# Kernel tuning notes

Hardware: AMD Instinct MI355X
Metric: run time of the kernel (lower is better)

Reference implementation:

```python
import jax, jax.numpy as jnp
import numpy as np

EPS = 1e-5
B, N, K = 2, 40960, 16
D_OUT = 64
H = D_OUT // 2  # 32

PNAMES = ['mlp1_w','mlp1_b','mlp1_g','mlp1_beta','mlp1_m','mlp1_v',
          'ap1_fc_w','ap1_fc_b','ap1_mlp_w','ap1_mlp_b','ap1_g','ap1_beta','ap1_m','ap1_v',
          'mlp2_w','mlp2_b','mlp2_g','mlp2_beta','mlp2_m','mlp2_v',
          'ap2_fc_w','ap2_fc_b','ap2_mlp_w','ap2_mlp_b','ap2_g','ap2_beta','ap2_m','ap2_v']


def _conv1x1(x, w, b):
    # x: (B,C,N,K), w: (O,C) -> (B,O,N,K)
    return jnp.einsum('oc,bcnk->bonk', w, x) + b[None, :, None, None]


def _bn(x, g, beta, m, v):
    # eval-mode BatchNorm2d over channel axis 1
    scale = g / jnp.sqrt(v + EPS)
    return (x - m[None, :, None, None]) * scale[None, :, None, None] + beta[None, :, None, None]


def _gather_neighbour(pc, idx):
    # pc: (B,N,d), idx: (B,N,K) -> (B,N,K,d)
    b, n, d = pc.shape
    k = idx.shape[-1]
    flat = idx.reshape(b, n * k)
    feats = jnp.take_along_axis(pc, flat[:, :, None], axis=1)  # (B,N*K,d)
    return feats.reshape(b, n, k, d)


def _rel_pos_enc(xyz, idx):
    nbr = _gather_neighbour(xyz, idx)                       # (B,N,K,3)
    tile = jnp.broadcast_to(xyz[:, :, None, :], nbr.shape)  # (B,N,K,3)
    rel = tile - nbr
    dist = jnp.sqrt(jnp.sum(rel * rel, axis=-1, keepdims=True))
    return jnp.concatenate([dist, rel, tile, nbr], axis=-1)  # (B,N,K,10)


def _att_pool(f, fc_w, fc_b, mw, mb, g, beta, m, v):
    # f: (B,C,N,K)
    att = jax.nn.relu(_conv1x1(f, fc_w, fc_b))
    scores = jax.nn.softmax(att, axis=3)
    agg = jnp.sum(f * scores, axis=3, keepdims=True)        # (B,C,N,1)
    return jax.nn.relu(_bn(_conv1x1(agg, mw, mb), g, beta, m, v))


def _forward(xyz, feature, neigh_idx, p):
    # relative pos encoding -> (B,10,N,K)
    f_xyz = _rel_pos_enc(xyz, neigh_idx).transpose(0, 3, 1, 2)
    f_xyz = jax.nn.relu(_bn(_conv1x1(f_xyz, p['mlp1_w'], p['mlp1_b']),
                            p['mlp1_g'], p['mlp1_beta'], p['mlp1_m'], p['mlp1_v']))  # (B,H,N,K)
    f_nb = _gather_neighbour(feature[..., 0].transpose(0, 2, 1), neigh_idx).transpose(0, 3, 1, 2)  # (B,H,N,K)
    f_cat = jnp.concatenate([f_nb, f_xyz], axis=1)          # (B,D_OUT,N,K)
    f_agg = _att_pool(f_cat, p['ap1_fc_w'], p['ap1_fc_b'], p['ap1_mlp_w'], p['ap1_mlp_b'],
                      p['ap1_g'], p['ap1_beta'], p['ap1_m'], p['ap1_v'])  # (B,H,N,1)
    f_xyz = jax.nn.relu(_bn(_conv1x1(f_xyz, p['mlp2_w'], p['mlp2_b']),
                            p['mlp2_g'], p['mlp2_beta'], p['mlp2_m'], p['mlp2_v']))  # (B,H,N,K)
    f_nb = _gather_neighbour(f_agg[..., 0].transpose(0, 2, 1), neigh_idx).transpose(0, 3, 1, 2)  # (B,H,N,K)
    f_cat = jnp.concatenate([f_nb, f_xyz], axis=1)          # (B,D_OUT,N,K)
    return _att_pool(f_cat, p['ap2_fc_w'], p['ap2_fc_b'], p['ap2_mlp_w'], p['ap2_mlp_b'],
                     p['ap2_g'], p['ap2_beta'], p['ap2_m'], p['ap2_v'])  # (B,D_OUT,N,1)


def setup_inputs() -> dict:
    key = jax.random.key(0)
    ks = iter(jax.random.split(key, 64))

    def w(o, c):
        return jax.random.normal(next(ks), (o, c), jnp.float32) * float(np.sqrt(2.0 / c))

    def bias(c):
        return jax.random.normal(next(ks), (c,), jnp.float32) * 0.01

    def bnp(c):
        g = jax.random.uniform(next(ks), (c,), jnp.float32, 0.5, 1.5)
        beta = jax.random.normal(next(ks), (c,), jnp.float32) * 0.1
        m = jax.random.normal(next(ks), (c,), jnp.float32) * 0.1
        v = jax.random.uniform(next(ks), (c,), jnp.float32, 0.5, 1.5)
        return g, beta, m, v

    inp = {}
    inp['xyz'] = jax.random.normal(next(ks), (B, N, 3), jnp.float32)
    inp['feature'] = jax.random.normal(next(ks), (B, H, N, 1), jnp.float32)
    inp['mlp1_w'], inp['mlp1_b'] = w(H, 10), bias(H)
    inp['mlp1_g'], inp['mlp1_beta'], inp['mlp1_m'], inp['mlp1_v'] = bnp(H)
    inp['ap1_fc_w'], inp['ap1_fc_b'] = w(D_OUT, D_OUT), bias(D_OUT)
    inp['ap1_mlp_w'], inp['ap1_mlp_b'] = w(H, D_OUT), bias(H)
    inp['ap1_g'], inp['ap1_beta'], inp['ap1_m'], inp['ap1_v'] = bnp(H)
    inp['mlp2_w'], inp['mlp2_b'] = w(H, H), bias(H)
    inp['mlp2_g'], inp['mlp2_beta'], inp['mlp2_m'], inp['mlp2_v'] = bnp(H)
    inp['ap2_fc_w'], inp['ap2_fc_b'] = w(D_OUT, D_OUT), bias(D_OUT)
    inp['ap2_mlp_w'], inp['ap2_mlp_b'] = w(D_OUT, D_OUT), bias(D_OUT)
    inp['ap2_g'], inp['ap2_beta'], inp['ap2_m'], inp['ap2_v'] = bnp(D_OUT)
    inp['neigh_idx'] = jax.random.randint(next(ks), (B, N, K), 0, N, jnp.int64 if jax.config.jax_enable_x64 else jnp.int32)
    return inp


def reference(xyz, feature, mlp1_w, mlp1_b, mlp1_g, mlp1_beta, mlp1_m, mlp1_v,
              ap1_fc_w, ap1_fc_b, ap1_mlp_w, ap1_mlp_b, ap1_g, ap1_beta, ap1_m, ap1_v,
              mlp2_w, mlp2_b, mlp2_g, mlp2_beta, mlp2_m, mlp2_v,
              ap2_fc_w, ap2_fc_b, ap2_mlp_w, ap2_mlp_b, ap2_g, ap2_beta, ap2_m, ap2_v,
              neigh_idx):
    p = dict(zip(PNAMES, (mlp1_w, mlp1_b, mlp1_g, mlp1_beta, mlp1_m, mlp1_v,
                          ap1_fc_w, ap1_fc_b, ap1_mlp_w, ap1_mlp_b, ap1_g, ap1_beta, ap1_m, ap1_v,
                          mlp2_w, mlp2_b, mlp2_g, mlp2_beta, mlp2_m, mlp2_v,
                          ap2_fc_w, ap2_fc_b, ap2_mlp_w, ap2_mlp_b, ap2_g, ap2_beta, ap2_m, ap2_v)))
    return _forward(xyz, feature, neigh_idx, p)
```

## Files before the change

kernel.cpp:

```cpp
#include <hip/hip_runtime.h>
#include <math.h>

#define BB 2
#define NN 40960
#define KK 16

typedef float v2f __attribute__((ext_vector_type(2)));
typedef _Float16 h16;
typedef h16 h16x2 __attribute__((ext_vector_type(2)));

__device__ __forceinline__ v2f fma2(v2f a, v2f b, v2f c){
  return __builtin_elementwise_fma(a, b, c);
}
__device__ __forceinline__ v2f mk2(float a, float b){ v2f r; r.x=a; r.y=b; return r; }

#if __has_builtin(__builtin_amdgcn_fdot2)
__device__ __forceinline__ float dot2acc(h16x2 w, h16x2 f, float acc){
  return __builtin_amdgcn_fdot2(w, f, acc, false);
}
#else
__device__ __forceinline__ float dot2acc(h16x2 w, h16x2 f, float acc){
  return acc + (float)w.x*(float)f.x + (float)w.y*(float)f.y;
}
#endif
#if __has_builtin(__builtin_amdgcn_exp2f)
__device__ __forceinline__ float exp2fast(float x){ return __builtin_amdgcn_exp2f(x); }
#else
__device__ __forceinline__ float exp2fast(float x){ return __expf(x*0.6931471805599453f); }
#endif
#if __has_builtin(__builtin_amdgcn_cvt_pkrtz)
__device__ __forceinline__ h16x2 pkh(float a, float b){
  return __builtin_bit_cast(h16x2, __builtin_amdgcn_cvt_pkrtz(a,b));
}
#else
__device__ __forceinline__ h16x2 pkh(float a, float b){ h16x2 r; r.x=(h16)a; r.y=(h16)b; return r; }
#endif

template<int CTRL>
__device__ __forceinline__ float dppf(float x){
  return __int_as_float(__builtin_amdgcn_update_dpp(0, __float_as_int(x), CTRL, 0xF, 0xF, true));
}
__device__ __forceinline__ float red16_sum(float v){
  v += dppf<0xB1>(v);
  v += dppf<0x4E>(v);
  v += dppf<0x141>(v);
  v += dppf<0x140>(v);
  return v;
}

__device__ alignas(16) float g_pw1[32*10];
__device__ alignas(16) float g_pb1[32];
__device__ alignas(16) h16x2 g_w2h[32*16];
__device__ alignas(16) float g_pb2[32];
__device__ alignas(16) h16x2 g_fch1[64*32];
__device__ alignas(16) float g_fcb1s[64];
__device__ alignas(16) h16x2 g_fch2[64*32];
__device__ alignas(16) float g_fcb2s[64];
__device__ alignas(16) float g_pcw[32*64];
__device__ alignas(16) float g_pcb[32];
__device__ alignas(16) float g_pdw[64*64];
__device__ alignas(16) float g_pdb[64];

#define LOG2E 1.44269504088896f

__global__ __launch_bounds__(256) void k_pre(
  const float* __restrict__ feat, float* __restrict__ feat_t,
  const float* __restrict__ w1, const float* __restrict__ b1,
  const float* __restrict__ g1, const float* __restrict__ be1, const float* __restrict__ m1, const float* __restrict__ v1,
  const float* __restrict__ fc1w, const float* __restrict__ fc1b,
  const float* __restrict__ cw, const float* __restrict__ cb,
  const float* __restrict__ cg, const float* __restrict__ cbe, const float* __restrict__ cm, const float* __restrict__ cv,
  const float* __restrict__ w2, const float* __restrict__ b2,
  const float* __restrict__ g2, const float* __restrict__ be2, const float* __restrict__ m2, const float* __restrict__ v2,
  const float* __restrict__ fc2w, const float* __restrict__ fc2b,
  const float* __restrict__ dw, const float* __restrict__ db,
  const float* __restrict__ dg, const float* __restrict__ dbe, const float* __restrict__ dm, const float* __restrict__ dv)
{
  int tid = threadIdx.x;
  int bid = blockIdx.x;
  if (bid < BB*NN/256){
    int b = bid / (NN/256);
    int n = (bid % (NN/256))*256 + tid;
    float v[32];
    #pragma unroll
    for (int h=0; h<32; ++h) v[h] = feat[((size_t)(b*32+h))*NN + n];
    float* o = feat_t + ((size_t)b*NN + n)*32;
    #pragma unroll
    for (int h=0; h<32; h+=4){ *(float4*)(o+h) = make_float4(v[h],v[h+1],v[h+2],v[h+3]); }
    return;
  }
  for (int i=tid; i<320; i+=256){ int h=i/10;
    g_pw1[i] = w1[i] * (g1[h]*rsqrtf(v1[h]+1e-5f)); }
  if (tid<32){ float s=g1[tid]*rsqrtf(v1[tid]+1e-5f);
    g_pb1[tid] = (b1[tid]-m1[tid])*s+be1[tid]; }
  for (int i=tid; i<512; i+=256){ int h=i>>4, c=i&15;
    float s=g2[h]*rsqrtf(v2[h]+1e-5f);
    g_w2h[i] = pkh(w2[h*32+2*c]*s, w2[h*32+2*c+1]*s); }
  if (tid<32){ float s=g2[tid]*rsqrtf(v2[tid]+1e-5f);
    g_pb2[tid] = (b2[tid]-m2[tid])*s+be2[tid]; }
  for (int i=tid; i<2048; i+=256){ int o=i>>5, c=i&31;
    g_fch1[i] = pkh(fc1w[o*64+2*c]*LOG2E, fc1w[o*64+2*c+1]*LOG2E);
    g_fch2[i] = pkh(fc2w[o*64+2*c]*LOG2E, fc2w[o*64+2*c+1]*LOG2E); }
  if (tid<64){ g_fcb1s[tid] = fc1b[tid]*LOG2E; g_fcb2s[tid] = fc2b[tid]*LOG2E; }
  for (int i=tid; i<2048; i+=256){ int h=i>>6;
    g_pcw[i] = cw[i] * (cg[h]*rsqrtf(cv[h]+1e-5f)); }
  if (tid<32){ float s=cg[tid]*rsqrtf(cv[tid]+1e-5f);
    g_pcb[tid] = (cb[tid]-cm[tid])*s+cbe[tid]; }
  for (int i=tid; i<4096; i+=256){ int h=i>>6;
    g_pdw[i] = dw[i] * (dg[h]*rsqrtf(dv[h]+1e-5f)); }
  if (tid<64){ float s=dg[tid]*rsqrtf(dv[tid]+1e-5f);
    g_pdb[tid] = (db[tid]-dm[tid])*s+dbe[tid]; }
}

__global__ __launch_bounds__(256,2) void k_stage1(
  const float* __restrict__ xyz, const float* __restrict__ feat_t, const int* __restrict__ nidx,
  float* __restrict__ fagg)
{
  int tid = threadIdx.x;
  int lane = tid & 63, wvv = tid >> 6;
  int k = lane & 15, ns = lane >> 4;
  int b = blockIdx.x / (NN/16);
  int n = (blockIdx.x % (NN/16))*16 + wvv*4 + ns;
  size_t bn = (size_t)b*NN + n;
  int idxv = nidx[bn*KK + k];

  alignas(16) float fc_[64];
  const float* fb = feat_t + ((size_t)b*NN + idxv)*32;
  #pragma unroll
  for (int h=0; h<32; h+=4){ float4 x=*(const float4*)(fb+h);
    fc_[h]=x.x; fc_[h+1]=x.y; fc_[h+2]=x.z; fc_[h+3]=x.w; }

  const float* tp = xyz + bn*3;
  const float* qp = xyz + ((size_t)b*NN + idxv)*3;
  float t0=tp[0],t1=tp[1],t2=tp[2];
  float q0=qp[0],q1=qp[1],q2=qp[2];
  float r0=t0-q0,r1=t1-q1,r2=t2-q2;
  v2f e2[5] = { {sqrtf(r0*r0+r1*r1+r2*r2), r0}, {r1,r2}, {t0,t1}, {t2,q0}, {q1,q2} };

  #pragma unroll
  for (int h=0; h<32; ++h){
    const v2f* wr = (const v2f*)(g_pw1 + h*10);
    v2f acc = mk2(g_pb1[h], 0.f);
    #pragma unroll
    for (int c=0; c<5; ++c) acc = fma2(wr[c], e2[c], acc);
    fc_[32+h] = fmaxf(acc.x+acc.y, 0.f);
  }

  h16x2 h2[32];
  #pragma unroll
  for (int c=0; c<32; ++c) h2[c] = pkh(fc_[2*c], fc_[2*c+1]);

  float sp4[4], sf4[4];
  #pragma unroll
  for (int ob=0; ob<64; ob+=4){
    const h16x2* w0 = &g_fch1[(ob+0)*32];
    const h16x2* w1p = &g_fch1[(ob+1)*32];
    const h16x2* w2p = &g_fch1[(ob+2)*32];
    const h16x2* w3p = &g_fch1[(ob+3)*32];
    float a0=g_fcb1s[ob+0], a1=g_fcb1s[ob+1], a2=g_fcb1s[ob+2], a3=g_fcb1s[ob+3];
    #pragma unroll
    for (int c=0; c<32; ++c){
      h16x2 f = h2[c];
      a0 = dot2acc(w0[c], f, a0); a1 = dot2acc(w1p[c], f, a1);
      a2 = dot2acc(w2p[c], f, a2); a3 = dot2acc(w3p[c], f, a3);
    }
    float p0=exp2fast(fmaxf(a0,0.f)), p1=exp2fast(fmaxf(a1,0.f));
    float p2=exp2fast(fmaxf(a2,0.f)), p3=exp2fast(fmaxf(a3,0.f));
    float f0=(float)h2[(ob>>1)+0].x, f1=(float)h2[(ob>>1)+0].y;
    float f2=(float)h2[(ob>>1)+1].x, f3=(float)h2[(ob>>1)+1].y;
    float q0v=f0*p0, q1v=f1*p1, q2v=f2*p2, q3v=f3*p3;
    float s0=red16_sum(p0), s1=red16_sum(p1), s2=red16_sum(p2), s3=red16_sum(p3);
    float t0v=red16_sum(q0v), t1v=red16_sum(q1v), t2v=red16_sum(q2v), t3v=red16_sum(q3v);
    if ((ob>>2)==k){
      sp4[0]=s0; sp4[1]=s1; sp4[2]=s2; sp4[3]=s3;
      sf4[0]=t0v; sf4[1]=t1v; sf4[2]=t2v; sf4[3]=t3v;
    }
  }
  v2f a01 = mk2(__fdividef(sf4[0],sp4[0]), __fdividef(sf4[1],sp4[1]));
  v2f a23 = mk2(__fdividef(sf4[2],sp4[2]), __fdividef(sf4[3],sp4[3]));

  float o0=0.f, o1=0.f;
  #pragma unroll
  for (int h=0; h<32; h+=2){
    const v2f* wr0 = (const v2f*)(g_pcw + h*64 + 4*k);
    const v2f* wr1 = (const v2f*)(g_pcw + (h+1)*64 + 4*k);
    v2f p0 = fma2(wr0[0], a01, wr0[1]*a23);
    v2f p1 = fma2(wr1[0], a01, wr1[1]*a23);
    float r0v = red16_sum(p0.x + p0.y);
    float r1v = red16_sum(p1.x + p1.y);
    float v0 = fmaxf(r0v + g_pcb[h], 0.f);
    float v1 = fmaxf(r1v + g_pcb[h+1], 0.f);
    if ((h&15)==k){ if (h<16) o0=v0; else o1=v0; }
    if (((h+1)&15)==k){ if (h+1<16) o0=v1; else o1=v1; }
  }
  float* fo = fagg + bn*32;
  fo[k]=o0; fo[k+16]=o1;
}

__global__ __launch_bounds__(256,2) void k_stage2(
  const float* __restrict__ xyz, const float* __restrict__ fagg, const int* __restrict__ nidx,
  float* __restrict__ outp)
{
  int tid = threadIdx.x;
  int lane = tid & 63, wvv = tid >> 6;
  int k = lane & 15, ns = lane >> 4;
  int b = blockIdx.x / (NN/16);
  int n = (blockIdx.x % (NN/16))*16 + wvv*4 + ns;
  size_t bn = (size_t)b*NN + n;
  int idxv = nidx[bn*KK + k];

  alignas(16) float fc_[64];
  const float* fb = fagg + ((size_t)b*NN + idxv)*32;
  #pragma unroll
  for (int h=0; h<32; h+=4){ float4 x=*(const float4*)(fb+h);
    fc_[h]=x.x; fc_[h+1]=x.y; fc_[h+2]=x.z; fc_[h+3]=x.w; }

  const float* tp = xyz + bn*3;
  const float* qp = xyz + ((size_t)b*NN + idxv)*3;
  float t0=tp[0],t1=tp[1],t2=tp[2];
  float q0=qp[0],q1=qp[1],q2=qp[2];
  float r0=t0-q0,r1=t1-q1,r2=t2-q2;
  v2f e2[5] = { {sqrtf(r0*r0+r1*r1+r2*r2), r0}, {r1,r2}, {t0,t1}, {t2,q0}, {q1,q2} };

  alignas(8) float fx[32];
  #pragma unroll
  for (int h=0; h<32; ++h){
    const v2f* wr = (const v2f*)(g_pw1 + h*10);
    v2f acc = mk2(g_pb1[h], 0.f);
    #pragma unroll
    for (int c=0; c<5; ++c) acc = fma2(wr[c], e2[c], acc);
    fx[h] = fmaxf(acc.x+acc.y, 0.f);
  }
  h16x2 hx[16];
  #pragma unroll
  for (int c=0; c<16; ++c) hx[c] = pkh(fx[2*c], fx[2*c+1]);
  #pragma unroll
  for (int h=0; h<32; h+=2){
    const h16x2* wr0 = &g_w2h[(h+0)*16];
    const h16x2* wr1 = &g_w2h[(h+1)*16];
    float a0 = g_pb2[h+0], a1 = g_pb2[h+1];
    #pragma unroll
    for (int c=0; c<16; ++c){ h16x2 f=hx[c]; a0=dot2acc(wr0[c],f,a0); a1=dot2acc(wr1[c],f,a1); }
    fc_[32+h]   = fmaxf(a0, 0.f);
    fc_[32+h+1] = fmaxf(a1, 0.f);
  }

  h16x2 h2[32];
  #pragma unroll
  for (int c=0; c<32; ++c) h2[c] = pkh(fc_[2*c], fc_[2*c+1]);

  float sp4[4], sf4[4];
  #pragma unroll
  for (int ob=0; ob<64; ob+=4){
    const h16x2* w0 = &g_fch2[(ob+0)*32];
    const h16x2* w1p = &g_fch2[(ob+1)*32];
    const h16x2* w2p = &g_fch2[(ob+2)*32];
    const h16x2* w3p = &g_fch2[(ob+3)*32];
    float a0=g_fcb2s[ob+0], a1=g_fcb2s[ob+1], a2=g_fcb2s[ob+2], a3=g_fcb2s[ob+3];
    #pragma unroll
    for (int c=0; c<32; ++c){
      h16x2 f = h2[c];
      a0 = dot2acc(w0[c], f, a0); a1 = dot2acc(w1p[c], f, a1);
      a2 = dot2acc(w2p[c], f, a2); a3 = dot2acc(w3p[c], f, a3);
    }
    float p0=exp2fast(fmaxf(a0,0.f)), p1=exp2fast(fmaxf(a1,0.f));
    float p2=exp2fast(fmaxf(a2,0.f)), p3=exp2fast(fmaxf(a3,0.f));
    float f0=(float)h2[(ob>>1)+0].x, f1=(float)h2[(ob>>1)+0].y;
    float f2=(float)h2[(ob>>1)+1].x, f3=(float)h2[(ob>>1)+1].y;
    float q0v=f0*p0, q1v=f1*p1, q2v=f2*p2, q3v=f3*p3;
    float s0=red16_sum(p0), s1=red16_sum(p1), s2=red16_sum(p2), s3=red16_sum(p3);
    float t0v=red16_sum(q0v), t1v=red16_sum(q1v), t2v=red16_sum(q2v), t3v=red16_sum(q3v);
    if ((ob>>2)==k){
      sp4[0]=s0; sp4[1]=s1; sp4[2]=s2; sp4[3]=s3;
      sf4[0]=t0v; sf4[1]=t1v; sf4[2]=t2v; sf4[3]=t3v;
    }
  }
  v2f a01 = mk2(__fdividef(sf4[0],sp4[0]), __fdividef(sf4[1],sp4[1]));
  v2f a23 = mk2(__fdividef(sf4[2],sp4[2]), __fdividef(sf4[3],sp4[3]));

  float o4[4];
  #pragma unroll
  for (int h=0; h<64; h+=2){
    const v2f* wr0 = (const v2f*)(g_pdw + h*64 + 4*k);
    const v2f* wr1 = (const v2f*)(g_pdw + (h+1)*64 + 4*k);
    v2f p0 = fma2(wr0[0], a01, wr0[1]*a23);
    v2f p1 = fma2(wr1[0], a01, wr1[1]*a23);
    float r0v = red16_sum(p0.x + p0.y);
    float r1v = red16_sum(p1.x + p1.y);
    float v0 = fmaxf(r0v + g_pdb[h], 0.f);
    float v1 = fmaxf(r1v + g_pdb[h+1], 0.f);
    if ((h&15)==k) o4[h>>4] = v0;
    if (((h+1)&15)==k) o4[(h+1)>>4] = v1;
  }
  #pragma unroll
  for (int j=0; j<4; ++j)
    outp[((size_t)(b*64 + k + 16*j))*NN + n] = o4[j];
}

extern "C" void kernel_launch(void* const* d_in, const int* in_sizes, int n_in,
                              void* d_out, int out_size, void* d_ws, size_t ws_size,
                              hipStream_t stream){
  const float* xyz     = (const float*)d_in[0];
  const float* feature = (const float*)d_in[1];
  const int*   nidx    = (const int*)d_in[30];
  float* feat_t = (float*)d_ws;
  float* fagg   = feat_t + (size_t)BB*NN*32;

  k_pre<<<BB*NN/256 + 1, 256, 0, stream>>>(feature, feat_t,
    (const float*)d_in[2],(const float*)d_in[3],(const float*)d_in[4],(const float*)d_in[5],
    (const float*)d_in[6],(const float*)d_in[7],
    (const float*)d_in[8],(const float*)d_in[9],
    (const float*)d_in[10],(const float*)d_in[11],(const float*)d_in[12],(const float*)d_in[13],
    (const float*)d_in[14],(const float*)d_in[15],
    (const float*)d_in[16],(const float*)d_in[17],(const float*)d_in[18],(const float*)d_in[19],
    (const float*)d_in[20],(const float*)d_in[21],
    (const float*)d_in[22],(const float*)d_in[23],
    (const float*)d_in[24],(const float*)d_in[25],(const float*)d_in[26],(const float*)d_in[27],
    (const float*)d_in[28],(const float*)d_in[29]);
  k_stage1<<<BB*NN/16, 256, 0, stream>>>(xyz, feat_t, nidx, fagg);
  k_stage2<<<BB*NN/16, 256, 0, stream>>>(xyz, fagg, nidx, (float*)d_out);
}
```

Baseline: 426.5 us.

## Replace DPP-reduced post-pool MLP with LDS broadcast and fp16 dot2 per-lane outputs

After attention pooling, each lane writes its four aggregated channels to shared memory. Every lane then reads back the full 64-channel vector and computes its own output channels with fp16 packed dot products. This replaces the earlier scheme of distributed partial products followed by 16-lane DPP reductions for every output channel. The post-pool weights are now stored as packed fp16, and features are packed to fp16 directly at load time. This cuts the many cross-lane reductions and register-array shuffling, but adds LDS traffic, a wave-level wait, and lower precision in the final matmul.

```diff
diff --git a/kernel.cpp b/kernel.cpp
--- a/kernel.cpp
+++ b/kernel.cpp
@@ -47,6 +47,10 @@
   v += dppf<0x140>(v);
   return v;
 }
+__device__ __forceinline__ void wave_sync(){
+  asm volatile("s_waitcnt lgkmcnt(0)" ::: "memory");
+  __builtin_amdgcn_sched_barrier(0);
+}
 
 __device__ alignas(16) float g_pw1[32*10];
 __device__ alignas(16) float g_pb1[32];
@@ -56,9 +60,9 @@
 __device__ alignas(16) float g_fcb1s[64];
 __device__ alignas(16) h16x2 g_fch2[64*32];
 __device__ alignas(16) float g_fcb2s[64];
-__device__ alignas(16) float g_pcw[32*64];
+__device__ alignas(16) h16x2 g_cwh[32*32];
 __device__ alignas(16) float g_pcb[32];
-__device__ alignas(16) float g_pdw[64*64];
+__device__ alignas(16) h16x2 g_dwh[64*32];
 __device__ alignas(16) float g_pdb[64];
 
 #define LOG2E 1.44269504088896f
@@ -102,12 +106,14 @@
     g_fch1[i] = pkh(fc1w[o*64+2*c]*LOG2E, fc1w[o*64+2*c+1]*LOG2E);
     g_fch2[i] = pkh(fc2w[o*64+2*c]*LOG2E, fc2w[o*64+2*c+1]*LOG2E); }
   if (tid<64){ g_fcb1s[tid] = fc1b[tid]*LOG2E; g_fcb2s[tid] = fc2b[tid]*LOG2E; }
-  for (int i=tid; i<2048; i+=256){ int h=i>>6;
-    g_pcw[i] = cw[i] * (cg[h]*rsqrtf(cv[h]+1e-5f)); }
+  for (int i=tid; i<1024; i+=256){ int h=i>>5, c=i&31;
+    float s=cg[h]*rsqrtf(cv[h]+1e-5f);
+    g_cwh[i] = pkh(cw[h*64+2*c]*s, cw[h*64+2*c+1]*s); }
   if (tid<32){ float s=cg[tid]*rsqrtf(cv[tid]+1e-5f);
     g_pcb[tid] = (cb[tid]-cm[tid])*s+cbe[tid]; }
-  for (int i=tid; i<4096; i+=256){ int h=i>>6;
-    g_pdw[i] = dw[i] * (dg[h]*rsqrtf(dv[h]+1e-5f)); }
+  for (int i=tid; i<2048; i+=256){ int o=i>>5, c=i&31;
+    float s=dg[o]*rsqrtf(dv[o]+1e-5f);
+    g_dwh[i] = pkh(dw[o*64+2*c]*s, dw[o*64+2*c+1]*s); }
   if (tid<64){ float s=dg[tid]*rsqrtf(dv[tid]+1e-5f);
     g_pdb[tid] = (db[tid]-dm[tid])*s+dbe[tid]; }
 }
@@ -116,6 +122,7 @@
   const float* __restrict__ xyz, const float* __restrict__ feat_t, const int* __restrict__ nidx,
   float* __restrict__ fagg)
 {
+  __shared__ float s_agg[4][4][64];
   int tid = threadIdx.x;
   int lane = tid & 63, wvv = tid >> 6;
   int k = lane & 15, ns = lane >> 4;
@@ -124,12 +131,13 @@
   size_t bn = (size_t)b*NN + n;
   int idxv = nidx[bn*KK + k];
 
-  alignas(16) float fc_[64];
-  const float* fb = feat_t + ((size_t)b*NN + idxv)*32;
-  #pragma unroll
-  for (int h=0; h<32; h+=4){ float4 x=*(const float4*)(fb+h);
-    fc_[h]=x.x; fc_[h+1]=x.y; fc_[h+2]=x.z; fc_[h+3]=x.w; }
-
+  h16x2 h2[32];
+  {
+    const float* fb = feat_t + ((size_t)b*NN + idxv)*32;
+    #pragma unroll
+    for (int h=0; h<32; h+=4){ float4 x=*(const float4*)(fb+h);
+      h2[h>>1] = pkh(x.x,x.y); h2[(h>>1)+1] = pkh(x.z,x.w); }
+  }
   const float* tp = xyz + bn*3;
   const float* qp = xyz + ((size_t)b*NN + idxv)*3;
   float t0=tp[0],t1=tp[1],t2=tp[2];
@@ -138,17 +146,14 @@
   v2f e2[5] = { {sqrtf(r0*r0+r1*r1+r2*r2), r0}, {r1,r2}, {t0,t1}, {t2,q0}, {q1,q2} };
 
   #pragma unroll
-  for (int h=0; h<32; ++h){
-    const v2f* wr = (const v2f*)(g_pw1 + h*10);
-    v2f acc = mk2(g_pb1[h], 0.f);
-    #pragma unroll
-    for (int c=0; c<5; ++c) acc = fma2(wr[c], e2[c], acc);
-    fc_[32+h] = fmaxf(acc.x+acc.y, 0.f);
-  }
-
-  h16x2 h2[32];
-  #pragma unroll
-  for (int c=0; c<32; ++c) h2[c] = pkh(fc_[2*c], fc_[2*c+1]);
+  for (int h=0; h<32; h+=2){
+    const v2f* w0 = (const v2f*)(g_pw1 + h*10);
+    const v2f* w1 = (const v2f*)(g_pw1 + (h+1)*10);
+    v2f a0=mk2(g_pb1[h],0.f), a1=mk2(g_pb1[h+1],0.f);
+    #pragma unroll
+    for (int c=0; c<5; ++c){ a0=fma2(w0[c],e2[c],a0); a1=fma2(w1[c],e2[c],a1); }
+    h2[16+(h>>1)] = pkh(fmaxf(a0.x+a0.y,0.f), fmaxf(a1.x+a1.y,0.f));
+  }
 
   float sp4[4], sf4[4];
   #pragma unroll
@@ -176,31 +181,33 @@
       sf4[0]=t0v; sf4[1]=t1v; sf4[2]=t2v; sf4[3]=t3v;
     }
   }
-  v2f a01 = mk2(__fdividef(sf4[0],sp4[0]), __fdividef(sf4[1],sp4[1]));
-  v2f a23 = mk2(__fdividef(sf4[2],sp4[2]), __fdividef(sf4[3],sp4[3]));
-
-  float o0=0.f, o1=0.f;
-  #pragma unroll
-  for (int h=0; h<32; h+=2){
-    const v2f* wr0 = (const v2f*)(g_pcw + h*64 + 4*k);
-    const v2f* wr1 = (const v2f*)(g_pcw + (h+1)*64 + 4*k);
-    v2f p0 = fma2(wr0[0], a01, wr0[1]*a23);
-    v2f p1 = fma2(wr1[0], a01, wr1[1]*a23);
-    float r0v = red16_sum(p0.x + p0.y);
-    float r1v = red16_sum(p1.x + p1.y);
-    float v0 = fmaxf(r0v + g_pcb[h], 0.f);
-    float v1 = fmaxf(r1v + g_pcb[h+1], 0.f);
-    if ((h&15)==k){ if (h<16) o0=v0; else o1=v0; }
-    if (((h+1)&15)==k){ if (h+1<16) o0=v1; else o1=v1; }
-  }
+  float a0=__fdividef(sf4[0],sp4[0]), a1=__fdividef(sf4[1],sp4[1]);
+  float a2=__fdividef(sf4[2],sp4[2]), a3=__fdividef(sf4[3],sp4[3]);
+
+  *(float4*)&s_agg[wvv][ns][4*k] = make_float4(a0,a1,a2,a3);
+  wave_sync();
+  h16x2 hAg[32];
+  {
+    const float* ag = &s_agg[wvv][ns][0];
+    #pragma unroll
+    for (int c4=0;c4<16;++c4){ float4 x = *(const float4*)(ag + 4*c4);
+      hAg[2*c4] = pkh(x.x,x.y); hAg[2*c4+1] = pkh(x.z,x.w); }
+  }
+  const h16x2* w0 = &g_cwh[k*32];
+  const h16x2* w1 = &g_cwh[(k+16)*32];
+  float o0 = g_pcb[k], o1 = g_pcb[k+16];
+  #pragma unroll
+  for (int c=0;c<32;++c){ o0 = dot2acc(w0[c], hAg[c], o0); o1 = dot2acc(w1[c], hAg[c], o1); }
   float* fo = fagg + bn*32;
-  fo[k]=o0; fo[k+16]=o1;
+  fo[k]    = fmaxf(o0, 0.f);
+  fo[k+16] = fmaxf(o1, 0.f);
 }
 
 __global__ __launch_bounds__(256,2) void k_stage2(
   const float* __restrict__ xyz, const float* __restrict__ fagg, const int* __restrict__ nidx,
   float* __restrict__ outp)
 {
+  __shared__ float s_agg[4][4][64];
   int tid = threadIdx.x;
   int lane = tid & 63, wvv = tid >> 6;
   int k = lane & 15, ns = lane >> 4;
@@ -209,12 +216,13 @@
   size_t bn = (size_t)b*NN + n;
   int idxv = nidx[bn*KK + k];
 
-  alignas(16) float fc_[64];
-  const float* fb = fagg + ((size_t)b*NN + idxv)*32;
-  #pragma unroll
-  for (int h=0; h<32; h+=4){ float4 x=*(const float4*)(fb+h);
-    fc_[h]=x.x; fc_[h+1]=x.y; fc_[h+2]=x.z; fc_[h+3]=x.w; }
-
+  h16x2 h2[32];
+  {
+    const float* fb = fagg + ((size_t)b*NN + idxv)*32;
+    #pragma unroll
+    for (int h=0; h<32; h+=4){ float4 x=*(const float4*)(fb+h);
+      h2[h>>1] = pkh(x.x,x.y); h2[(h>>1)+1] = pkh(x.z,x.w); }
+  }
   const float* tp = xyz + bn*3;
   const float* qp = xyz + ((size_t)b*NN + idxv)*3;
   float t0=tp[0],t1=tp[1],t2=tp[2];
@@ -222,18 +230,16 @@
   float r0=t0-q0,r1=t1-q1,r2=t2-q2;
   v2f e2[5] = { {sqrtf(r0*r0+r1*r1+r2*r2), r0}, {r1,r2}, {t0,t1}, {t2,q0}, {q1,q2} };
 
-  alignas(8) float fx[32];
-  #pragma unroll
-  for (int h=0; h<32; ++h){
-    const v2f* wr = (const v2f*)(g_pw1 + h*10);
-    v2f acc = mk2(g_pb1[h], 0.f);
-    #pragma unroll
-    for (int c=0; c<5; ++c) acc = fma2(wr[c], e2[c], acc);
-    fx[h] = fmaxf(acc.x+acc.y, 0.f);
-  }
   h16x2 hx[16];
   #pragma unroll
-  for (int c=0; c<16; ++c) hx[c] = pkh(fx[2*c], fx[2*c+1]);
+  for (int h=0; h<32; h+=2){
+    const v2f* w0 = (const v2f*)(g_pw1 + h*10);
+    const v2f* w1 = (const v2f*)(g_pw1 + (h+1)*10);
+    v2f a0=mk2(g_pb1[h],0.f), a1=mk2(g_pb1[h+1],0.f);
+    #pragma unroll
+    for (int c=0; c<5; ++c){ a0=fma2(w0[c],e2[c],a0); a1=fma2(w1[c],e2[c],a1); }
+    hx[h>>1] = pkh(fmaxf(a0.x+a0.y,0.f), fmaxf(a1.x+a1.y,0.f));
+  }
   #pragma unroll
   for (int h=0; h<32; h+=2){
     const h16x2* wr0 = &g_w2h[(h+0)*16];
@@ -241,13 +247,8 @@
     float a0 = g_pb2[h+0], a1 = g_pb2[h+1];
     #pragma unroll
     for (int c=0; c<16; ++c){ h16x2 f=hx[c]; a0=dot2acc(wr0[c],f,a0); a1=dot2acc(wr1[c],f,a1); }
-    fc_[32+h]   = fmaxf(a0, 0.f);
-    fc_[32+h+1] = fmaxf(a1, 0.f);
-  }
-
-  h16x2 h2[32];
-  #pragma unroll
-  for (int c=0; c<32; ++c) h2[c] = pkh(fc_[2*c], fc_[2*c+1]);
+    h2[16+(h>>1)] = pkh(fmaxf(a0,0.f), fmaxf(a1,0.f));
+  }
 
   float sp4[4], sf4[4];
   #pragma unroll
@@ -275,26 +276,26 @@
       sf4[0]=t0v; sf4[1]=t1v; sf4[2]=t2v; sf4[3]=t3v;
     }
   }
-  v2f a01 = mk2(__fdividef(sf4[0],sp4[0]), __fdividef(sf4[1],sp4[1]));
-  v2f a23 = mk2(__fdividef(sf4[2],sp4[2]), __fdividef(sf4[3],sp4[3]));
-
-  float o4[4];
-  #pragma unroll
-  for (int h=0; h<64; h+=2){
-    const v2f* wr0 = (const v2f*)(g_pdw + h*64 + 4*k);
-    const v2f* wr1 = (const v2f*)(g_pdw + (h+1)*64 + 4*k);
-    v2f p0 = fma2(wr0[0], a01, wr0[1]*a23);
-    v2f p1 = fma2(wr1[0], a01, wr1[1]*a23);
-    float r0v = red16_sum(p0.x + p0.y);
-    float r1v = red16_sum(p1.x + p1.y);
-    float v0 = fmaxf(r0v + g_pdb[h], 0.f);
-    float v1 = fmaxf(r1v + g_pdb[h+1], 0.f);
-    if ((h&15)==k) o4[h>>4] = v0;
-    if (((h+1)&15)==k) o4[(h+1)>>4] = v1;
-  }
-  #pragma unroll
-  for (int j=0; j<4; ++j)
-    outp[((size_t)(b*64 + k + 16*j))*NN + n] = o4[j];
+  float a0=__fdividef(sf4[0],sp4[0]), a1=__fdividef(sf4[1],sp4[1]);
+  float a2=__fdividef(sf4[2],sp4[2]), a3=__fdividef(sf4[3],sp4[3]);
+
+  *(float4*)&s_agg[wvv][ns][4*k] = make_float4(a0,a1,a2,a3);
+  wave_sync();
+  h16x2 hAg[32];
+  {
+    const float* ag = &s_agg[wvv][ns][0];
+    #pragma unroll
+    for (int c4=0;c4<16;++c4){ float4 x = *(const float4*)(ag + 4*c4);
+      hAg[2*c4] = pkh(x.x,x.y); hAg[2*c4+1] = pkh(x.z,x.w); }
+  }
+  #pragma unroll
+  for (int j=0; j<4; ++j){
+    const h16x2* wr = &g_dwh[(k+16*j)*32];
+    float acc = g_pdb[k+16*j];
+    #pragma unroll
+    for (int c=0;c<32;++c) acc = dot2acc(wr[c], hAg[c], acc);
+    outp[((size_t)(b*64 + k + 16*j))*NN + n] = fmaxf(acc, 0.f);
+  }
 }
 
 extern "C" void kernel_launch(void* const* d_in, const int* in_sizes, int n_in,
```

Result: faster. 407.6 us (-4.4%).
